# Kernel optimization log

Measured on AMD Instinct MI355X. Metric: run time of the kernel, lower is better.

The kernel has to match this reference:

```python
import jax, jax.numpy as jnp
import numpy as np

N = 10000
NEG_SLOPE = 0.2

def _glorot(key, shape):
    fan = shape[0] + shape[-1]
    return jax.random.normal(key, shape, dtype=jnp.float32) * jnp.sqrt(2.0 / fan)

def gat_conv(x, src, dst, W, a_src, a_dst, b, heads, ch, concat, n):
    # PyG GATConv: linear (no bias), per-head attention logits, softmax over
    # incoming edges of each target node, weighted scatter-sum, final bias.
    h = (x @ W).reshape(n, heads, ch)                     # [N,H,C]
    al_s = jnp.einsum('nhc,hc->nh', h, a_src)             # [N,H]
    al_d = jnp.einsum('nhc,hc->nh', h, a_dst)
    e = jax.nn.leaky_relu(al_s[src] + al_d[dst], NEG_SLOPE)  # [E,H]
    emax = jax.ops.segment_max(e, dst, num_segments=n)    # [N,H]
    emax = jnp.where(jnp.isfinite(emax), emax, 0.0)
    p = jnp.exp(e - emax[dst])
    denom = jax.ops.segment_sum(p, dst, num_segments=n)   # [N,H]
    alpha = p / (denom[dst] + 1e-16)                      # [E,H]
    out = jax.ops.segment_sum(h[src] * alpha[:, :, None], dst, num_segments=n)
    out = out.reshape(n, heads * ch) if concat else out.mean(axis=1)
    return out + b

def _with_self_loops(edge_index, n):
    loop = jnp.arange(n, dtype=edge_index.dtype)
    src = jnp.concatenate([edge_index[0], loop])
    dst = jnp.concatenate([edge_index[1], loop])
    return src, dst

def setup_inputs() -> dict:
    key = jax.random.key(0)
    ks = jax.random.split(key, 20)
    in_dim, out_dim, E = 128, 256, 160000
    x = jax.random.normal(ks[0], (N, in_dim), dtype=jnp.float32)
    edge_index = jax.random.randint(ks[1], (2, E), 0, N, dtype=jnp.int64)
    return {
        'x': x, 'edge_index': edge_index,
        # conv1: GATConv(128, 256, heads=4, concat=True)
        'W1': _glorot(ks[2], (in_dim, 4 * 256)),
        'a1s': _glorot(ks[3], (4, 256)), 'a1d': _glorot(ks[4], (4, 256)),
        'b1': jnp.zeros((1024,), jnp.float32),
        'S1w': _glorot(ks[5], (in_dim, 1024)), 'S1b': jnp.zeros((1024,), jnp.float32),
        # conv2: GATConv(1024, 256, heads=4, concat=True)
        'W2': _glorot(ks[6], (1024, 4 * 256)),
        'a2s': _glorot(ks[7], (4, 256)), 'a2d': _glorot(ks[8], (4, 256)),
        'b2': jnp.zeros((1024,), jnp.float32),
        'S2w': _glorot(ks[9], (1024, 1024)), 'S2b': jnp.zeros((1024,), jnp.float32),
        # conv3: GATConv(1024, 256, heads=6, concat=False)
        'W3': _glorot(ks[10], (1024, 6 * out_dim)),
        'a3s': _glorot(ks[11], (6, out_dim)), 'a3d': _glorot(ks[12], (6, out_dim)),
        'b3': jnp.zeros((out_dim,), jnp.float32),
        'S3w': _glorot(ks[13], (1024, out_dim)), 'S3b': jnp.zeros((out_dim,), jnp.float32),
    }

def reference(x, edge_index, W1, a1s, a1d, b1, S1w, S1b,
              W2, a2s, a2d, b2, S2w, S2b,
              W3, a3s, a3d, b3, S3w, S3b):
    src, dst = _with_self_loops(edge_index, N)
    h = jax.nn.elu(gat_conv(x, src, dst, W1, a1s, a1d, b1, 4, 256, True, N) + x @ S1w + S1b)
    h = jax.nn.elu(gat_conv(h, src, dst, W2, a2s, a2d, b2, 4, 256, True, N) + h @ S2w + S2b)
    out = gat_conv(h, src, dst, W3, a3s, a3d, b3, 6, 256, False, N) + h @ S3w + S3b
    return out
```

## Files before the change

### kernel.cpp

```cpp
#include <hip/hip_runtime.h>
#include <cfloat>
#include <cmath>
#include <cstdint>

#define NN 10000
#define EE 160000
#define ETOT 170000
#define MPAD 10240

typedef _Float16 f16;
typedef __attribute__((ext_vector_type(8))) _Float16 f16x8;
typedef __attribute__((ext_vector_type(4))) float f32x4;

__global__ __launch_bounds__(256) void count_deg_k(const int* __restrict__ ei,
                                                   int* __restrict__ deg) {
    int e = blockIdx.x * 256 + threadIdx.x;
    if (e < ETOT) {
        int dst = (e < EE) ? ei[EE + e] : (e - EE);
        atomicAdd(&deg[dst], 1);
    }
}

__global__ __launch_bounds__(256) void sc1_k(const int* __restrict__ deg,
                                             int* __restrict__ tmp,
                                             int* __restrict__ bsum) {
    __shared__ int s[256];
    int i = blockIdx.x * 256 + threadIdx.x;
    int v = (i < NN) ? deg[i] : 0;
    s[threadIdx.x] = v;
    __syncthreads();
    for (int d = 1; d < 256; d <<= 1) {
        int t = (threadIdx.x >= d) ? s[threadIdx.x - d] : 0;
        __syncthreads();
        s[threadIdx.x] += t;
        __syncthreads();
    }
    if (i < NN) tmp[i] = s[threadIdx.x];
    if (threadIdx.x == 255) bsum[blockIdx.x] = s[255];
}

__global__ __launch_bounds__(64) void sc2_k(const int* __restrict__ bsum,
                                            int* __restrict__ bbase) {
    int lane = threadIdx.x;
    int v = (lane < 40) ? bsum[lane] : 0;
    int incl = v;
    for (int d = 1; d < 64; d <<= 1) {
        int t = __shfl_up(incl, d, 64);
        if (lane >= d) incl += t;
    }
    if (lane < 40) bbase[lane] = incl - v;
}

__global__ __launch_bounds__(256) void sc3_k(const int* __restrict__ deg,
                                             const int* __restrict__ tmp,
                                             const int* __restrict__ bbase,
                                             int* __restrict__ offs,
                                             int* __restrict__ pos) {
    int i = blockIdx.x * 256 + threadIdx.x;
    if (i < NN) {
        int incl = tmp[i] + bbase[blockIdx.x];
        offs[i + 1] = incl;
        pos[i]      = incl - deg[i];
    }
    if (i == 0) offs[0] = 0;
}

__global__ __launch_bounds__(256) void scatter_k(const int* __restrict__ ei,
                                                 int* __restrict__ pos,
                                                 int* __restrict__ esrc) {
    int e = blockIdx.x * 256 + threadIdx.x;
    if (e < ETOT) {
        int dst = (e < EE) ? ei[EE + e] : (e - EE);
        int src = (e < EE) ? ei[e]      : (e - EE);
        int p = atomicAdd(&pos[dst], 1);
        esrc[p] = src;
    }
}

__device__ __forceinline__ int swz(int r, int ko) { return ko ^ ((r >> 1) & 3); }

template <bool DOELU>
__global__ __launch_bounds__(256) void convA_k(const float* __restrict__ A,
                                               f16* __restrict__ Adst,
                                               int M, int K, int kshift) {
    int idx = blockIdx.x * 256 + threadIdx.x;
    int row = idx >> kshift;
    int kc  = idx & ((1 << kshift) - 1);
    float v[8];
    if (row < M) {
        const float* p = A + (size_t)row * K + kc * 8;
        float4 f0 = *(const float4*)p, f1 = *(const float4*)(p + 4);
        v[0]=f0.x; v[1]=f0.y; v[2]=f0.z; v[3]=f0.w;
        v[4]=f1.x; v[5]=f1.y; v[6]=f1.z; v[7]=f1.w;
        if (DOELU) {
#pragma unroll
            for (int i = 0; i < 8; i++) v[i] = (v[i] > 0.f) ? v[i] : expf(v[i]) - 1.f;
        }
    } else {
#pragma unroll
        for (int i = 0; i < 8; i++) v[i] = 0.f;
    }
    int mblk = row >> 7, r = row & 127;
    int kblk = kc >> 2,  ko = kc & 3;
    int KB = K >> 5, KB2 = KB * 2;
    size_t inoff = r * 32 + swz(r, ko) * 8;
    f16x8 h, l;
#pragma unroll
    for (int i = 0; i < 8; i++) {
        f16 hv = (f16)v[i];
        h[i] = hv;
        l[i] = (f16)(v[i] - (float)hv);
    }
    *(f16x8*)(Adst + (size_t)(mblk * KB2 + kblk) * 4096 + inoff)      = h;
    *(f16x8*)(Adst + (size_t)(mblk * KB2 + KB + kblk) * 4096 + inoff) = l;
}

__global__ __launch_bounds__(256) void convB_k(const float* __restrict__ B,
                                               f16* __restrict__ Bdst,
                                               int NcSrc, int colOff, int KB) {
    int n  = blockIdx.x * 256 + threadIdx.x;
    int kc = blockIdx.y;
    const float* p = B + (size_t)(kc * 8) * NcSrc + n;
    int gcol = colOff + n;
    int nblk = gcol >> 7, r = gcol & 127;
    int kblk = kc >> 2,  ko = kc & 3;
    int KB2 = KB * 2;
    size_t inoff = r * 32 + swz(r, ko) * 8;
    f16x8 h;
#pragma unroll
    for (int i = 0; i < 8; i++) h[i] = (f16)p[(size_t)i * NcSrc];
    *(f16x8*)(Bdst + (size_t)(nblk * KB2 + kblk) * 4096 + inoff)      = h;
    *(f16x8*)(Bdst + (size_t)(nblk * KB2 + KB + kblk) * 4096 + inoff) = h;
}

__device__ __forceinline__ void gl_lds16(const void* g, void* l) {
    __builtin_amdgcn_global_load_lds(
        (const __attribute__((address_space(1))) uint32_t*)g,
        (__attribute__((address_space(3))) uint32_t*)l, 16, 0, 0);
}

__global__ __launch_bounds__(512) void mm_k(const f16* __restrict__ Ap,
                                            const f16* __restrict__ Bp,
                                            float* __restrict__ C2,
                                            f16* __restrict__ C1h,
                                            const float* __restrict__ bias1,
                                            const float* __restrict__ bias2,
                                            const float* __restrict__ a_s,
                                            const float* __restrict__ a_d,
                                            float* __restrict__ als,
                                            float* __restrict__ ald,
                                            int M, int KB2, int NB1,
                                            int N1, int N2, int H) {
    __shared__ __align__(16) char lds[49152];
    const int tid = threadIdx.x;
    const int mblk = blockIdx.y, nblk = blockIdx.x;
    const int lane = tid & 63, w = tid >> 6;
    const int wr = w >> 1, wc = w & 1;
    const int kg = lane >> 4, l15 = lane & 15;

    int offA[2][4], offB[2][4];
#pragma unroll
    for (int t = 0; t < 4; t++) {
        int ra = wr * 64 + t * 16 + l15;
        int s = ra >> 7, r = ra & 127;
        int rb = wc * 64 + t * 16 + l15;
#pragma unroll
        for (int hh = 0; hh < 2; hh++) {
            offA[hh][t] = hh * 16384 + s * 8192 + r * 64 + swz(r, kg) * 16;
            offB[hh][t] = 32768 + hh * 8192 + rb * 64 + swz(rb, kg) * 16;
        }
    }

    const char* gA = (const char*)Ap;
    const char* gB = (const char*)Bp + (size_t)nblk * KB2 * 8192;

    f32x4 acc[4][4];
#pragma unroll
    for (int i = 0; i < 4; i++)
#pragma unroll
        for (int j = 0; j < 4; j++) acc[i][j] = (f32x4){0.f, 0.f, 0.f, 0.f};

    const int nsteps = KB2 >> 1;
    for (int kb = 0; kb < nsteps; kb++) {
        const int t16 = tid * 16;
#pragma unroll
        for (int hh = 0; hh < 2; hh++) {
            int kt = 2 * kb + hh;
#pragma unroll
            for (int s = 0; s < 2; s++)
                gl_lds16(gA + ((size_t)((2 * mblk + s) * KB2 + kt)) * 8192 + t16,
                         lds + hh * 16384 + s * 8192 + t16);
            gl_lds16(gB + (size_t)kt * 8192 + t16, lds + 32768 + hh * 8192 + t16);
        }
        __syncthreads();

#pragma unroll
        for (int hh = 0; hh < 2; hh++) {
            f16x8 a[4], b[4];
#pragma unroll
            for (int t = 0; t < 4; t++) {
                a[t] = *(const f16x8*)(lds + offA[hh][t]);
                b[t] = *(const f16x8*)(lds + offB[hh][t]);
            }
#pragma unroll
            for (int i = 0; i < 4; i++)
#pragma unroll
                for (int j = 0; j < 4; j++)
                    acc[i][j] = __builtin_amdgcn_mfma_f32_16x16x32_f16(a[i], b[j], acc[i][j], 0, 0, 0);
        }
        __syncthreads();
    }

    const int rowBase = mblk * 256 + wr * 64;
    const int colBase = nblk * 128 + wc * 64;
    if (nblk < NB1) {
#pragma unroll
        for (int i = 0; i < 4; i++)
#pragma unroll
            for (int j = 0; j < 4; j++) {
                int col = colBase + j * 16 + l15;
#pragma unroll
                for (int q = 0; q < 4; q++) {
                    int row = rowBase + i * 16 + kg * 4 + q;
                    C1h[(size_t)row * N1 + col] = (f16)acc[i][j][q];
                }
            }
        const int head = nblk >> 1;
        const int cIn  = (nblk & 1) * 128 + wc * 64;
        float asv[4], adv[4];
#pragma unroll
        for (int j = 0; j < 4; j++) {
            asv[j] = a_s[head * 256 + cIn + j * 16 + l15];
            adv[j] = a_d[head * 256 + cIn + j * 16 + l15];
        }
#pragma unroll
        for (int i = 0; i < 4; i++)
#pragma unroll
            for (int q = 0; q < 4; q++) {
                float vs = acc[i][0][q] * asv[0] + acc[i][1][q] * asv[1]
                         + acc[i][2][q] * asv[2] + acc[i][3][q] * asv[3];
                float vd = acc[i][0][q] * adv[0] + acc[i][1][q] * adv[1]
                         + acc[i][2][q] * adv[2] + acc[i][3][q] * adv[3];
                vs += __shfl_xor(vs, 1); vs += __shfl_xor(vs, 2);
                vs += __shfl_xor(vs, 4); vs += __shfl_xor(vs, 8);
                vd += __shfl_xor(vd, 1); vd += __shfl_xor(vd, 2);
                vd += __shfl_xor(vd, 4); vd += __shfl_xor(vd, 8);
                if (l15 == 0) {
                    int row = rowBase + i * 16 + kg * 4 + q;
                    if (row < M) {
                        atomicAdd(&als[row * H + head], vs);
                        atomicAdd(&ald[row * H + head], vd);
                    }
                }
            }
    } else {
        const int cb2 = NB1 * 128;
#pragma unroll
        for (int i = 0; i < 4; i++)
#pragma unroll
            for (int j = 0; j < 4; j++) {
                int c2 = colBase + j * 16 + l15 - cb2;
                float bsum = bias1[c2] + bias2[c2];
#pragma unroll
                for (int q = 0; q < 4; q++) {
                    int row = rowBase + i * 16 + kg * 4 + q;
                    if (row < M) C2[(size_t)row * N2 + c2] = acc[i][j][q] + bsum;
                }
            }
    }
}

template <int H, bool MEAN>
__global__ __launch_bounds__(256) void smagg_k(const int* __restrict__ offs,
                                               const int* __restrict__ esrc,
                                               const float* __restrict__ als,
                                               const float* __restrict__ ald,
                                               const f16* __restrict__ hfeat16,
                                               float* __restrict__ out) {
    constexpr int NC = H * 256;
    __shared__ float s_l[128 * 9];
    __shared__ float s_p[128 * 9];
    __shared__ int   s_src[128];
    __shared__ float s_m[8], s_s[8], s_scale[8], s_ad[8];

    const int n = blockIdx.x;
    const int tid = threadIdx.x;
    const int base = offs[n], cnt = offs[n + 1] - base;

    if (tid < H) {
        s_m[tid] = -1e30f;
        s_s[tid] = 0.f;
        s_ad[tid] = ald[n * H + tid];
    }
    float acc[H];
#pragma unroll
    for (int h = 0; h < H; h++) acc[h] = 0.f;
    __syncthreads();

    for (int c0 = 0; c0 < cnt; c0 += 128) {
        const int mcnt = min(128, cnt - c0);
        if (tid < mcnt) {
            int src = esrc[base + c0 + tid];
            s_src[tid] = src;
#pragma unroll
            for (int h = 0; h < H; h++) {
                float l = als[src * H + h] + s_ad[h];
                l = (l < 0.f) ? 0.2f * l : l;
                s_l[tid * 9 + h] = l;
            }
        }
        __syncthreads();
        if (tid < H * 32) {
            int h = tid >> 5, l5 = tid & 31;
            float m = -1e30f;
            for (int e = l5; e < mcnt; e += 32) m = fmaxf(m, s_l[e * 9 + h]);
            for (int o = 16; o > 0; o >>= 1) m = fmaxf(m, __shfl_xor(m, o, 32));
            float mNew = fmaxf(s_m[h], m);
            float ssum = 0.f;
            for (int e = l5; e < mcnt; e += 32) ssum += __expf(s_l[e * 9 + h] - mNew);
            for (int o = 16; o > 0; o >>= 1) ssum += __shfl_xor(ssum, o, 32);
            if (l5 == 0) {
                float scale = __expf(s_m[h] - mNew);
                s_scale[h] = scale;
                s_s[h] = s_s[h] * scale + ssum;
                s_m[h] = mNew;
            }
        }
        __syncthreads();
        if (tid < mcnt) {
#pragma unroll
            for (int h = 0; h < H; h++)
                s_p[tid * 9 + h] = __expf(s_l[tid * 9 + h] - s_m[h]);
        }
#pragma unroll
        for (int h = 0; h < H; h++) acc[h] *= s_scale[h];
        __syncthreads();
        for (int e = 0; e < mcnt; e++) {
            const f16* hp = hfeat16 + (size_t)s_src[e] * NC + tid;
#pragma unroll
            for (int h = 0; h < H; h++)
                acc[h] += s_p[e * 9 + h] * (float)hp[h * 256];
        }
        __syncthreads();
    }

    if (MEAN) {
        float v = 0.f;
#pragma unroll
        for (int h = 0; h < H; h++) v += acc[h] / (s_s[h] + 1e-16f);
        out[(size_t)n * 256 + tid] += v * (1.f / 6.f);
    } else {
#pragma unroll
        for (int h = 0; h < H; h++)
            out[(size_t)n * NC + h * 256 + tid] += acc[h] / (s_s[h] + 1e-16f);
    }
}

extern "C" void kernel_launch(void* const* d_in, const int* in_sizes, int n_in,
                              void* d_out, int out_size, void* d_ws, size_t ws_size,
                              hipStream_t stream) {
    const float* x   = (const float*)d_in[0];
    const int*   ei  = (const int*)d_in[1];
    const float* W1  = (const float*)d_in[2];
    const float* a1s = (const float*)d_in[3];
    const float* a1d = (const float*)d_in[4];
    const float* b1  = (const float*)d_in[5];
    const float* S1w = (const float*)d_in[6];
    const float* S1b = (const float*)d_in[7];
    const float* W2  = (const float*)d_in[8];
    const float* a2s = (const float*)d_in[9];
    const float* a2d = (const float*)d_in[10];
    const float* b2  = (const float*)d_in[11];
    const float* S2w = (const float*)d_in[12];
    const float* S2b = (const float*)d_in[13];
    const float* W3  = (const float*)d_in[14];
    const float* a3s = (const float*)d_in[15];
    const float* a3d = (const float*)d_in[16];
    const float* b3  = (const float*)d_in[17];
    const float* S3w = (const float*)d_in[18];
    const float* S3b = (const float*)d_in[19];
    float* out = (float*)d_out;

    float* ws = (float*)d_ws;
    size_t o = 0;
    float* bufA = ws + o; o += (size_t)NN * 1024;
    float* bufB = ws + o; o += (size_t)NN * 1024;
    float* als  = ws + o; o += (size_t)NN * 6;
    float* ald  = ws + o; o += (size_t)NN * 6;
    f16* hfeat16 = (f16*)(ws + o); o += (size_t)MPAD * 1536 / 2;
    f16* At  = (f16*)(ws + o); o += (size_t)MPAD * 2048 / 2;
    f16* Bt1 = (f16*)(ws + o); o += (size_t)16 * 8  * 4096 / 2;
    f16* Bt2 = (f16*)(ws + o); o += (size_t)16 * 64 * 4096 / 2;
    f16* Bt3 = (f16*)(ws + o); o += (size_t)14 * 64 * 4096 / 2;
    int* deg   = (int*)(ws + o);
    int* tmp   = deg + NN;
    int* bsum  = tmp + NN;
    int* bbase = bsum + 64;
    int* offs  = bbase + 64;
    int* pos   = offs + NN + 1;
    int* esrc  = pos + NN;

    hipMemsetAsync(deg, 0, NN * sizeof(int), stream);
    count_deg_k<<<(ETOT + 255) / 256, 256, 0, stream>>>(ei, deg);
    sc1_k<<<40, 256, 0, stream>>>(deg, tmp, bsum);
    sc2_k<<<1, 64, 0, stream>>>(bsum, bbase);
    sc3_k<<<40, 256, 0, stream>>>(deg, tmp, bbase, offs, pos);
    scatter_k<<<(ETOT + 255) / 256, 256, 0, stream>>>(ei, pos, esrc);

    convB_k<<<dim3(4, 16),  256, 0, stream>>>(W1,  Bt1, 1024, 0,    4);
    convB_k<<<dim3(4, 16),  256, 0, stream>>>(S1w, Bt1, 1024, 1024, 4);
    convB_k<<<dim3(4, 128), 256, 0, stream>>>(W2,  Bt2, 1024, 0,    32);
    convB_k<<<dim3(4, 128), 256, 0, stream>>>(S2w, Bt2, 1024, 1024, 32);
    convB_k<<<dim3(6, 128), 256, 0, stream>>>(W3,  Bt3, 1536, 0,    32);
    convB_k<<<dim3(1, 128), 256, 0, stream>>>(S3w, Bt3, 256,  1536, 32);

    convA_k<false><<<MPAD * 16 / 256, 256, 0, stream>>>(x, At, NN, 128, 4);
    hipMemsetAsync(als, 0, NN * 12 * sizeof(float), stream);
    mm_k<<<dim3(16, 40), 512, 0, stream>>>(At, Bt1, bufA, hfeat16, S1b, b1,
                                           a1s, a1d, als, ald,
                                           NN, 8, 8, 1024, 1024, 4);
    smagg_k<4, false><<<NN, 256, 0, stream>>>(offs, esrc, als, ald, hfeat16, bufA);

    convA_k<true><<<MPAD * 128 / 256, 256, 0, stream>>>(bufA, At, NN, 1024, 7);
    hipMemsetAsync(als, 0, NN * 12 * sizeof(float), stream);
    mm_k<<<dim3(16, 40), 512, 0, stream>>>(At, Bt2, bufB, hfeat16, S2b, b2,
                                           a2s, a2d, als, ald,
                                           NN, 64, 8, 1024, 1024, 4);
    smagg_k<4, false><<<NN, 256, 0, stream>>>(offs, esrc, als, ald, hfeat16, bufB);

    convA_k<true><<<MPAD * 128 / 256, 256, 0, stream>>>(bufB, At, NN, 1024, 7);
    hipMemsetAsync(als, 0, NN * 12 * sizeof(float), stream);
    mm_k<<<dim3(14, 40), 512, 0, stream>>>(At, Bt3, out, hfeat16, S3b, b3,
                                           a3s, a3d, als, ald,
                                           NN, 64, 12, 1536, 256, 6);
    smagg_k<6, true><<<NN, 256, 0, stream>>>(offs, esrc, als, ald, hfeat16, out);
}
```

Baseline: 663.5 us.

## Split A hi/lo buffers, shrink GEMM tile to 128x128, add XCD-aware block remap

Splits the fp16 hi/lo halves of A into separate buffers and stops duplicating B, so each K step loads A-hi, A-lo and one B tile and issues two MFMAs per output fragment. The GEMM drops from 512-thread 256x128 tiles to 256-thread 128x128 tiles with half the LDS, doubling the grid along M and trimming the M padding. A block-index remap groups consecutive tiles onto the same XCD to improve L2 locality. Smaller tiles mean less reuse of each B load but better occupancy and a better balance of blocks across CUs.

Measured after the change: 646.3 us. 1.03x faster.

```diff
diff --git a/kernel.cpp b/kernel.cpp
--- a/kernel.cpp
+++ b/kernel.cpp
@@ -6,7 +6,7 @@
 #define NN 10000
 #define EE 160000
 #define ETOT 170000
-#define MPAD 10240
+#define MPAD 10112
 
 typedef _Float16 f16;
 typedef __attribute__((ext_vector_type(8))) _Float16 f16x8;
@@ -81,7 +81,8 @@
 
 template <bool DOELU>
 __global__ __launch_bounds__(256) void convA_k(const float* __restrict__ A,
-                                               f16* __restrict__ Adst,
+                                               f16* __restrict__ hi,
+                                               f16* __restrict__ lo,
                                                int M, int K, int kshift) {
     int idx = blockIdx.x * 256 + threadIdx.x;
     int row = idx >> kshift;
@@ -102,8 +103,8 @@
     }
     int mblk = row >> 7, r = row & 127;
     int kblk = kc >> 2,  ko = kc & 3;
-    int KB = K >> 5, KB2 = KB * 2;
-    size_t inoff = r * 32 + swz(r, ko) * 8;
+    int KB = K >> 5;
+    size_t off = ((size_t)(mblk * KB + kblk)) * 4096 + r * 32 + swz(r, ko) * 8;
     f16x8 h, l;
 #pragma unroll
     for (int i = 0; i < 8; i++) {
@@ -111,8 +112,8 @@
         h[i] = hv;
         l[i] = (f16)(v[i] - (float)hv);
     }
-    *(f16x8*)(Adst + (size_t)(mblk * KB2 + kblk) * 4096 + inoff)      = h;
-    *(f16x8*)(Adst + (size_t)(mblk * KB2 + KB + kblk) * 4096 + inoff) = l;
+    *(f16x8*)(hi + off) = h;
+    *(f16x8*)(lo + off) = l;
 }
 
 __global__ __launch_bounds__(256) void convB_k(const float* __restrict__ B,
@@ -124,13 +125,11 @@
     int gcol = colOff + n;
     int nblk = gcol >> 7, r = gcol & 127;
     int kblk = kc >> 2,  ko = kc & 3;
-    int KB2 = KB * 2;
-    size_t inoff = r * 32 + swz(r, ko) * 8;
+    size_t off = ((size_t)(nblk * KB + kblk)) * 4096 + r * 32 + swz(r, ko) * 8;
     f16x8 h;
 #pragma unroll
     for (int i = 0; i < 8; i++) h[i] = (f16)p[(size_t)i * NcSrc];
-    *(f16x8*)(Bdst + (size_t)(nblk * KB2 + kblk) * 4096 + inoff)      = h;
-    *(f16x8*)(Bdst + (size_t)(nblk * KB2 + KB + kblk) * 4096 + inoff) = h;
+    *(f16x8*)(Bdst + off) = h;
 }
 
 __device__ __forceinline__ void gl_lds16(const void* g, void* l) {
@@ -139,8 +138,9 @@
         (__attribute__((address_space(3))) uint32_t*)l, 16, 0, 0);
 }
 
-__global__ __launch_bounds__(512) void mm_k(const f16* __restrict__ Ap,
-                                            const f16* __restrict__ Bp,
+__global__ __launch_bounds__(256) void mm_k(const f16* __restrict__ Ahi,
+                                            const f16* __restrict__ Alo,
+                                            const f16* __restrict__ Bhi,
                                             float* __restrict__ C2,
                                             f16* __restrict__ C1h,
                                             const float* __restrict__ bias1,
@@ -149,30 +149,34 @@
                                             const float* __restrict__ a_d,
                                             float* __restrict__ als,
                                             float* __restrict__ ald,
-                                            int M, int KB2, int NB1,
+                                            int M, int KB, int NB1,
                                             int N1, int N2, int H) {
-    __shared__ __align__(16) char lds[49152];
+    __shared__ __align__(16) char lds[24576];
     const int tid = threadIdx.x;
-    const int mblk = blockIdx.y, nblk = blockIdx.x;
+
+    const int nwg  = gridDim.x * gridDim.y;
+    const int orig = blockIdx.y * gridDim.x + blockIdx.x;
+    const int q = nwg >> 3, rr = nwg & 7;
+    const int xcd = orig & 7, rk = orig >> 3;
+    const int lin = (xcd < rr ? xcd * (q + 1) : rr * (q + 1) + (xcd - rr) * q) + rk;
+    const int mblk = lin / gridDim.x, nblk = lin % gridDim.x;
+
     const int lane = tid & 63, w = tid >> 6;
     const int wr = w >> 1, wc = w & 1;
     const int kg = lane >> 4, l15 = lane & 15;
 
-    int offA[2][4], offB[2][4];
+    int offA[4], offB[4];
 #pragma unroll
     for (int t = 0; t < 4; t++) {
         int ra = wr * 64 + t * 16 + l15;
-        int s = ra >> 7, r = ra & 127;
+        offA[t] = ra * 64 + swz(ra, kg) * 16;
         int rb = wc * 64 + t * 16 + l15;
-#pragma unroll
-        for (int hh = 0; hh < 2; hh++) {
-            offA[hh][t] = hh * 16384 + s * 8192 + r * 64 + swz(r, kg) * 16;
-            offB[hh][t] = 32768 + hh * 8192 + rb * 64 + swz(rb, kg) * 16;
-        }
-    }
-
-    const char* gA = (const char*)Ap;
-    const char* gB = (const char*)Bp + (size_t)nblk * KB2 * 8192;
+        offB[t] = 16384 + rb * 64 + swz(rb, kg) * 16;
+    }
+
+    const char* gAh = (const char*)Ahi + (size_t)mblk * KB * 8192;
+    const char* gAl = (const char*)Alo + (size_t)mblk * KB * 8192;
+    const char* gBh = (const char*)Bhi + (size_t)nblk * KB * 8192;
 
     f32x4 acc[4][4];
 #pragma unroll
@@ -180,38 +184,35 @@
 #pragma unroll
         for (int j = 0; j < 4; j++) acc[i][j] = (f32x4){0.f, 0.f, 0.f, 0.f};
 
-    const int nsteps = KB2 >> 1;
-    for (int kb = 0; kb < nsteps; kb++) {
+    for (int kb = 0; kb < KB; kb++) {
+        const size_t tk = (size_t)kb * 8192;
         const int t16 = tid * 16;
-#pragma unroll
-        for (int hh = 0; hh < 2; hh++) {
-            int kt = 2 * kb + hh;
-#pragma unroll
-            for (int s = 0; s < 2; s++)
-                gl_lds16(gA + ((size_t)((2 * mblk + s) * KB2 + kt)) * 8192 + t16,
-                         lds + hh * 16384 + s * 8192 + t16);
-            gl_lds16(gB + (size_t)kt * 8192 + t16, lds + 32768 + hh * 8192 + t16);
-        }
-        __syncthreads();
-
-#pragma unroll
-        for (int hh = 0; hh < 2; hh++) {
-            f16x8 a[4], b[4];
-#pragma unroll
-            for (int t = 0; t < 4; t++) {
-                a[t] = *(const f16x8*)(lds + offA[hh][t]);
-                b[t] = *(const f16x8*)(lds + offB[hh][t]);
-            }
-#pragma unroll
-            for (int i = 0; i < 4; i++)
-#pragma unroll
-                for (int j = 0; j < 4; j++)
-                    acc[i][j] = __builtin_amdgcn_mfma_f32_16x16x32_f16(a[i], b[j], acc[i][j], 0, 0, 0);
-        }
-        __syncthreads();
-    }
-
-    const int rowBase = mblk * 256 + wr * 64;
+        gl_lds16(gAh + tk + t16,        lds + t16);
+        gl_lds16(gAh + tk + 4096 + t16, lds + 4096 + t16);
+        gl_lds16(gAl + tk + t16,        lds + 8192 + t16);
+        gl_lds16(gAl + tk + 4096 + t16, lds + 12288 + t16);
+        gl_lds16(gBh + tk + t16,        lds + 16384 + t16);
+        gl_lds16(gBh + tk + 4096 + t16, lds + 20480 + t16);
+        __syncthreads();
+
+        f16x8 ah[4], al[4], b[4];
+#pragma unroll
+        for (int t = 0; t < 4; t++) {
+            ah[t] = *(const f16x8*)(lds + offA[t]);
+            al[t] = *(const f16x8*)(lds + 8192 + offA[t]);
+            b[t]  = *(const f16x8*)(lds + offB[t]);
+        }
+#pragma unroll
+        for (int i = 0; i < 4; i++)
+#pragma unroll
+            for (int j = 0; j < 4; j++) {
+                acc[i][j] = __builtin_amdgcn_mfma_f32_16x16x32_f16(ah[i], b[j], acc[i][j], 0, 0, 0);
+                acc[i][j] = __builtin_amdgcn_mfma_f32_16x16x32_f16(al[i], b[j], acc[i][j], 0, 0, 0);
+            }
+        __syncthreads();
+    }
+
+    const int rowBase = mblk * 128 + wr * 64;
     const int colBase = nblk * 128 + wc * 64;
     if (nblk < NB1) {
 #pragma unroll
@@ -220,9 +221,9 @@
             for (int j = 0; j < 4; j++) {
                 int col = colBase + j * 16 + l15;
 #pragma unroll
-                for (int q = 0; q < 4; q++) {
-                    int row = rowBase + i * 16 + kg * 4 + q;
-                    C1h[(size_t)row * N1 + col] = (f16)acc[i][j][q];
+                for (int q2 = 0; q2 < 4; q2++) {
+                    int row = rowBase + i * 16 + kg * 4 + q2;
+                    C1h[(size_t)row * N1 + col] = (f16)acc[i][j][q2];
                 }
             }
         const int head = nblk >> 1;
@@ -236,17 +237,17 @@
 #pragma unroll
         for (int i = 0; i < 4; i++)
 #pragma unroll
-            for (int q = 0; q < 4; q++) {
-                float vs = acc[i][0][q] * asv[0] + acc[i][1][q] * asv[1]
-                         + acc[i][2][q] * asv[2] + acc[i][3][q] * asv[3];
-                float vd = acc[i][0][q] * adv[0] + acc[i][1][q] * adv[1]
-                         + acc[i][2][q] * adv[2] + acc[i][3][q] * adv[3];
+            for (int q2 = 0; q2 < 4; q2++) {
+                float vs = acc[i][0][q2] * asv[0] + acc[i][1][q2] * asv[1]
+                         + acc[i][2][q2] * asv[2] + acc[i][3][q2] * asv[3];
+                float vd = acc[i][0][q2] * adv[0] + acc[i][1][q2] * adv[1]
+                         + acc[i][2][q2] * adv[2] + acc[i][3][q2] * adv[3];
                 vs += __shfl_xor(vs, 1); vs += __shfl_xor(vs, 2);
                 vs += __shfl_xor(vs, 4); vs += __shfl_xor(vs, 8);
                 vd += __shfl_xor(vd, 1); vd += __shfl_xor(vd, 2);
                 vd += __shfl_xor(vd, 4); vd += __shfl_xor(vd, 8);
                 if (l15 == 0) {
-                    int row = rowBase + i * 16 + kg * 4 + q;
+                    int row = rowBase + i * 16 + kg * 4 + q2;
                     if (row < M) {
                         atomicAdd(&als[row * H + head], vs);
                         atomicAdd(&ald[row * H + head], vd);
@@ -262,9 +263,9 @@
                 int c2 = colBase + j * 16 + l15 - cb2;
                 float bsum = bias1[c2] + bias2[c2];
 #pragma unroll
-                for (int q = 0; q < 4; q++) {
-                    int row = rowBase + i * 16 + kg * 4 + q;
-                    if (row < M) C2[(size_t)row * N2 + c2] = acc[i][j][q] + bsum;
+                for (int q2 = 0; q2 < 4; q2++) {
+                    int row = rowBase + i * 16 + kg * 4 + q2;
+                    if (row < M) C2[(size_t)row * N2 + c2] = acc[i][j][q2] + bsum;
                 }
             }
     }
@@ -388,10 +389,11 @@
     float* als  = ws + o; o += (size_t)NN * 6;
     float* ald  = ws + o; o += (size_t)NN * 6;
     f16* hfeat16 = (f16*)(ws + o); o += (size_t)MPAD * 1536 / 2;
-    f16* At  = (f16*)(ws + o); o += (size_t)MPAD * 2048 / 2;
-    f16* Bt1 = (f16*)(ws + o); o += (size_t)16 * 8  * 4096 / 2;
-    f16* Bt2 = (f16*)(ws + o); o += (size_t)16 * 64 * 4096 / 2;
-    f16* Bt3 = (f16*)(ws + o); o += (size_t)14 * 64 * 4096 / 2;
+    f16* AhiT = (f16*)(ws + o); o += (size_t)MPAD * 1024 / 2;
+    f16* AloT = (f16*)(ws + o); o += (size_t)MPAD * 1024 / 2;
+    f16* Bt1  = (f16*)(ws + o); o += (size_t)16 * 4  * 4096 / 2;
+    f16* Bt2  = (f16*)(ws + o); o += (size_t)16 * 32 * 4096 / 2;
+    f16* Bt3  = (f16*)(ws + o); o += (size_t)14 * 32 * 4096 / 2;
     int* deg   = (int*)(ws + o);
     int* tmp   = deg + NN;
     int* bsum  = tmp + NN;
@@ -414,24 +416,24 @@
     convB_k<<<dim3(6, 128), 256, 0, stream>>>(W3,  Bt3, 1536, 0,    32);
     convB_k<<<dim3(1, 128), 256, 0, stream>>>(S3w, Bt3, 256,  1536, 32);
 
-    convA_k<false><<<MPAD * 16 / 256, 256, 0, stream>>>(x, At, NN, 128, 4);
+    convA_k<false><<<MPAD * 16 / 256, 256, 0, stream>>>(x, AhiT, AloT, NN, 128, 4);
     hipMemsetAsync(als, 0, NN * 12 * sizeof(float), stream);
-    mm_k<<<dim3(16, 40), 512, 0, stream>>>(At, Bt1, bufA, hfeat16, S1b, b1,
+    mm_k<<<dim3(16, 79), 256, 0, stream>>>(AhiT, AloT, Bt1, bufA, hfeat16, S1b, b1,
                                            a1s, a1d, als, ald,
-                                           NN, 8, 8, 1024, 1024, 4);
+                                           NN, 4, 8, 1024, 1024, 4);
     smagg_k<4, false><<<NN, 256, 0, stream>>>(offs, esrc, als, ald, hfeat16, bufA);
 
-    convA_k<true><<<MPAD * 128 / 256, 256, 0, stream>>>(bufA, At, NN, 1024, 7);
+    convA_k<true><<<MPAD * 128 / 256, 256, 0, stream>>>(bufA, AhiT, AloT, NN, 1024, 7);
     hipMemsetAsync(als, 0, NN * 12 * sizeof(float), stream);
-    mm_k<<<dim3(16, 40), 512, 0, stream>>>(At, Bt2, bufB, hfeat16, S2b, b2,
+    mm_k<<<dim3(16, 79), 256, 0, stream>>>(AhiT, AloT, Bt2, bufB, hfeat16, S2b, b2,
                                            a2s, a2d, als, ald,
-                                           NN, 64, 8, 1024, 1024, 4);
+                                           NN, 32, 8, 1024, 1024, 4);
     smagg_k<4, false><<<NN, 256, 0, stream>>>(offs, esrc, als, ald, hfeat16, bufB);
 
-    convA_k<true><<<MPAD * 128 / 256, 256, 0, stream>>>(bufB, At, NN, 1024, 7);
+    convA_k<true><<<MPAD * 128 / 256, 256, 0, stream>>>(bufB, AhiT, AloT, NN, 1024, 7);
     hipMemsetAsync(als, 0, NN * 12 * sizeof(float), stream);
-    mm_k<<<dim3(14, 40), 512, 0, stream>>>(At, Bt3, out, hfeat16, S3b, b3,
+    mm_k<<<dim3(14, 79), 256, 0, stream>>>(AhiT, AloT, Bt3, out, hfeat16, S3b, b3,
                                            a3s, a3d, als, ald,
-                                           NN, 64, 12, 1536, 256, 6);
+                                           NN, 32, 12, 1536, 256, 6);
     smagg_k<6, true><<<NN, 256, 0, stream>>>(offs, esrc, als, ald, hfeat16, out);
 }
```
